# Kernel tuning notes

Measured on AMD Instinct MI355X. Metric: run time of the kernel, lower is better.

Reference implementation:

```python
import jax, jax.numpy as jnp
import numpy as np

F_SIZE = 3
Z_DIM = 128
IN_CH = 1024
OUT_CH = 8
FEAT = 32          # feature_size
NZ = FEAT * FEAT   # 1024


def setup_inputs() -> dict:
    key = jax.random.key(0)
    k_z, k_wi, k_bi, k_wo, k_bo = jax.random.split(key, 5)
    s_in = 1.0 / np.sqrt(NZ)
    s_out = 1.0 / np.sqrt(Z_DIM)
    return {
        "z": jax.random.normal(k_z, (IN_CH, FEAT, FEAT), dtype=jnp.float32),
        # stacked per-channel Linear(Nz -> z_dim): weight (C, z_dim, Nz), bias (C, z_dim)
        "W_in": jax.random.uniform(k_wi, (IN_CH, Z_DIM, NZ), jnp.float32, -s_in, s_in),
        "b_in": jax.random.uniform(k_bi, (IN_CH, Z_DIM), jnp.float32, -s_in, s_in),
        # shared Linear(z_dim -> out_ch*f*f)
        "W_out": jax.random.uniform(k_wo, (OUT_CH * F_SIZE * F_SIZE, Z_DIM), jnp.float32, -s_out, s_out),
        "b_out": jax.random.uniform(k_bo, (OUT_CH * F_SIZE * F_SIZE,), jnp.float32, -s_out, s_out),
    }


def reference(z, W_in, b_in, W_out, b_out):
    C, h, w = z.shape
    x = z.reshape(C, h * w)                              # (C, Nz) per-channel flattened latent
    a = jnp.einsum('cdn,cn->cd', W_in, x) + b_in          # batched per-channel GEMV: (C, z_dim)
    k = a @ W_out.T + b_out                               # shared linear: (C, out_ch*f*f)
    # each channel's k viewed as (out_ch, 1, f, f), concatenated along dim=1
    K = k.reshape(C, OUT_CH, F_SIZE, F_SIZE).transpose(1, 0, 2, 3)  # (out_ch, C, f, f)
    return K
```

## Files before the change

### kernel.cpp

```cpp
#include <hip/hip_runtime.h>

#define NCH   1024
#define ZDIM  128
#define NZ    1024
#define KOUT  72

__global__ __launch_bounds__(256, 4) void hyper_fused_kernel(
    const float* __restrict__ z,
    const float* __restrict__ W_in,
    const float* __restrict__ b_in,
    const float* __restrict__ W_out,
    const float* __restrict__ b_out,
    float* __restrict__ out)
{
    __shared__ float xs[NZ];
    __shared__ float as[ZDIM];

    const int c    = blockIdx.x;
    const int tid  = threadIdx.x;
    const int lane = tid & 63;
    const int wave = tid >> 6;

    const float4* zp  = (const float4*)(z + (size_t)c * NZ);
    float4*       xs4 = (float4*)xs;
    xs4[tid] = zp[tid];
    __syncthreads();

    const float4* Wc = (const float4*)(W_in + (size_t)c * ZDIM * NZ);
    for (int dd = 0; dd < 32; ++dd) {
        const int d = wave * 32 + dd;
        const float4* row = Wc + (size_t)d * (NZ / 4);
        float sum = 0.f;
        #pragma unroll
        for (int k = 0; k < 4; ++k) {
            const float4 wv = row[lane + 64 * k];
            const float4 xv = xs4[lane + 64 * k];
            sum += wv.x * xv.x + wv.y * xv.y + wv.z * xv.z + wv.w * xv.w;
        }
        #pragma unroll
        for (int off = 32; off > 0; off >>= 1)
            sum += __shfl_xor(sum, off, 64);
        if (lane == 0)
            as[d] = sum + b_in[c * ZDIM + d];
    }
    __syncthreads();

    if (tid < KOUT) {
        const float4* wr = (const float4*)(W_out + tid * ZDIM);
        const float4* av = (const float4*)as;
        float sum = 0.f;
        #pragma unroll
        for (int j = 0; j < ZDIM / 4; ++j) {
            const float4 w = wr[j];
            const float4 a = av[j];
            sum += w.x * a.x + w.y * a.y + w.z * a.z + w.w * a.w;
        }
        sum += b_out[tid];
        const int o = tid / 9;
        const int r = tid % 9;
        out[(size_t)o * (NCH * 9) + (size_t)c * 9 + r] = sum;
    }
}

extern "C" void kernel_launch(void* const* d_in, const int* in_sizes, int n_in,
                              void* d_out, int out_size, void* d_ws, size_t ws_size,
                              hipStream_t stream) {
    const float* z     = (const float*)d_in[0];
    const float* W_in  = (const float*)d_in[1];
    const float* b_in  = (const float*)d_in[2];
    const float* W_out = (const float*)d_in[3];
    const float* b_out = (const float*)d_in[4];
    float* out = (float*)d_out;

    hyper_fused_kernel<<<NCH, 256, 0, stream>>>(z, W_in, b_in, W_out, b_out, out);
}
```

Measured before the change: 105.0 us.

## Keep latent in registers, stream W_in with nontemporal loads, process two rows per iteration

Each wave now loads the channel's latent vector straight into registers instead of staging it through shared memory, which removes the initial barrier and the LDS reads. W_in rows are read two at a time with nontemporal loads so more memory requests are in flight and the single-use weights do not pollute the cache. The two row reductions share one shuffle tree after a first combining step. Register pressure rises from holding the latent and eight weight vectors at once.

```diff
diff --git a/kernel.cpp b/kernel.cpp
--- a/kernel.cpp
+++ b/kernel.cpp
@@ -4,6 +4,12 @@
 #define ZDIM  128
 #define NZ    1024
 #define KOUT  72
+
+typedef float f4 __attribute__((ext_vector_type(4)));
+
+__device__ __forceinline__ float dot4(f4 a, f4 b) {
+    return a.x * b.x + a.y * b.y + a.z * b.z + a.w * b.w;
+}
 
 __global__ __launch_bounds__(256, 4) void hyper_fused_kernel(
     const float* __restrict__ z,
@@ -13,7 +19,6 @@
     const float* __restrict__ b_out,
     float* __restrict__ out)
 {
-    __shared__ float xs[NZ];
     __shared__ float as[ZDIM];
 
     const int c    = blockIdx.x;
@@ -21,40 +26,53 @@
     const int lane = tid & 63;
     const int wave = tid >> 6;
 
-    const float4* zp  = (const float4*)(z + (size_t)c * NZ);
-    float4*       xs4 = (float4*)xs;
-    xs4[tid] = zp[tid];
-    __syncthreads();
+    const f4* zp = (const f4*)(z + (size_t)c * NZ);
+    const f4 xv0 = zp[lane];
+    const f4 xv1 = zp[lane + 64];
+    const f4 xv2 = zp[lane + 128];
+    const f4 xv3 = zp[lane + 192];
 
-    const float4* Wc = (const float4*)(W_in + (size_t)c * ZDIM * NZ);
-    for (int dd = 0; dd < 32; ++dd) {
-        const int d = wave * 32 + dd;
-        const float4* row = Wc + (size_t)d * (NZ / 4);
-        float sum = 0.f;
-        #pragma unroll
-        for (int k = 0; k < 4; ++k) {
-            const float4 wv = row[lane + 64 * k];
-            const float4 xv = xs4[lane + 64 * k];
-            sum += wv.x * xv.x + wv.y * xv.y + wv.z * xv.z + wv.w * xv.w;
-        }
-        #pragma unroll
-        for (int off = 32; off > 0; off >>= 1)
-            sum += __shfl_xor(sum, off, 64);
-        if (lane == 0)
-            as[d] = sum + b_in[c * ZDIM + d];
+    const f4* Wc = (const f4*)(W_in + (size_t)c * ZDIM * NZ);
+    const float* bc = b_in + c * ZDIM;
+
+    for (int dd = 0; dd < 32; dd += 2) {
+        const int d0 = wave * 32 + dd;
+        const f4* r0 = Wc + (size_t)d0 * (NZ / 4) + lane;
+        const f4* r1 = r0 + (NZ / 4);
+
+        const f4 a0 = __builtin_nontemporal_load(r0);
+        const f4 a1 = __builtin_nontemporal_load(r0 + 64);
+        const f4 a2 = __builtin_nontemporal_load(r0 + 128);
+        const f4 a3 = __builtin_nontemporal_load(r0 + 192);
+        const f4 b0 = __builtin_nontemporal_load(r1);
+        const f4 b1 = __builtin_nontemporal_load(r1 + 64);
+        const f4 b2 = __builtin_nontemporal_load(r1 + 128);
+        const f4 b3 = __builtin_nontemporal_load(r1 + 192);
+
+        float s0 = dot4(a0, xv0) + dot4(a1, xv1) + dot4(a2, xv2) + dot4(a3, xv3);
+        float s1 = dot4(b0, xv0) + dot4(b1, xv1) + dot4(b2, xv2) + dot4(b3, xv3);
+
+        float t0 = s0 + __shfl_xor(s0, 32, 64);
+        float t1 = s1 + __shfl_xor(s1, 32, 64);
+        float u  = (lane < 32) ? t0 : t1;
+        u += __shfl_xor(u, 16, 64);
+        u += __shfl_xor(u, 8, 64);
+        u += __shfl_xor(u, 4, 64);
+        u += __shfl_xor(u, 2, 64);
+        u += __shfl_xor(u, 1, 64);
+
+        if (lane == 0)  as[d0]     = u + bc[d0];
+        if (lane == 32) as[d0 + 1] = u + bc[d0 + 1];
     }
     __syncthreads();
 
     if (tid < KOUT) {
-        const float4* wr = (const float4*)(W_out + tid * ZDIM);
-        const float4* av = (const float4*)as;
+        const f4* wr = (const f4*)(W_out + tid * ZDIM);
+        const f4* av = (const f4*)as;
         float sum = 0.f;
         #pragma unroll
-        for (int j = 0; j < ZDIM / 4; ++j) {
-            const float4 w = wr[j];
-            const float4 a = av[j];
-            sum += w.x * a.x + w.y * a.y + w.z * a.z + w.w * a.w;
-        }
+        for (int j = 0; j < ZDIM / 4; ++j)
+            sum += dot4(wr[j], av[j]);
         sum += b_out[tid];
         const int o = tid / 9;
         const int r = tid % 9;
```

Measured after the change: 96.63 us. -8.0%, faster.
